# Kernel optimization log

Measured on AMD Instinct MI355X. Metric: run time of the kernel, lower is better.

## Reference

```python
import jax, jax.numpy as jnp
import numpy as np

B, T, D = 2, 2048, 1024
H, K = 16, 64  # num_heads, key_size (value_size == key_size)


def setup_inputs() -> dict:
    key = jax.random.key(0)
    ks = jax.random.split(key, 9)
    # xavier-uniform-ish scale for square-ish projections
    def xavier(k, shape):
        fan_in, fan_out = shape[0], shape[1]
        lim = jnp.sqrt(6.0 / (fan_in + fan_out))
        return jax.random.uniform(k, shape, jnp.float32, -lim, lim)
    return {
        "x_q": jax.random.normal(ks[0], (B, T, D), jnp.float32),
        "Wq": xavier(ks[1], (D, H * K)),
        "bq": jnp.zeros((H * K,), jnp.float32),
        "Wk": xavier(ks[2], (D, H * K)),
        "bk": jnp.zeros((H * K,), jnp.float32),
        "Wv": xavier(ks[3], (D, H * K)),
        "bv": jnp.zeros((H * K,), jnp.float32),
        "Wo": xavier(ks[4], (H * K, D)),
        "bo": jnp.zeros((D,), jnp.float32),
    }


def reference(x_q, Wq, bq, Wk, bk, Wv, bv, Wo, bo):
    # self-attention: x_k = x_v = x_q
    q = (x_q @ Wq + bq).reshape(B, T, H, K)
    k = (x_q @ Wk + bk).reshape(B, T, H, K)
    v = (x_q @ Wv + bv).reshape(B, T, H, K)
    # dense_dot_product_attention, mask=None
    logits = jnp.einsum('bqhd,bkhd->bhqk', q, k) / jnp.sqrt(jnp.asarray(K, k.dtype))
    attn_w = jax.nn.softmax(logits, axis=-1)  # [B,H,Tq,Tk]
    attn = jnp.einsum('bhqk,bkhd->bqhd', attn_w, v).reshape(B, T, H * K)
    out = attn @ Wo + bo  # [B,T,D]
    return out
```

## Files before the change

### kernel.cpp

```cpp
#include <hip/hip_runtime.h>
#include <hip/hip_bf16.h>
#include <stdint.h>

#define B_  2
#define T_  2048
#define D_  1024
#define H_  16
#define KS  64
#define M_  (B_*T_)

typedef unsigned short u16;
typedef __bf16 bf16x8 __attribute__((ext_vector_type(8)));
typedef __bf16 bf16x4 __attribute__((ext_vector_type(4)));
typedef float  f32x4  __attribute__((ext_vector_type(4)));

#define AS1 __attribute__((address_space(1)))
#define AS3 __attribute__((address_space(3)))

__device__ inline u16 f2bf(float x){
  union { float f; uint32_t u; } v; v.f = x;
  uint32_t r = (v.u + 0x7fffu + ((v.u >> 16) & 1u)) >> 16;
  return (u16)r;
}

__device__ inline void gl_lds16(const u16* g, u16* l){
  __builtin_amdgcn_global_load_lds((AS1 void*)(const_cast<u16*>(g)),
                                   (AS3 void*)l, 16, 0, 0);
}

__global__ __launch_bounds__(256) void k_cvt_x(const float* __restrict__ x,
                                               u16* __restrict__ xb){
  int i = blockIdx.x * 256 + threadIdx.x;
  float4 v = ((const float4*)x)[i];
  ushort4 o;
  o.x = f2bf(v.x); o.y = f2bf(v.y); o.z = f2bf(v.z); o.w = f2bf(v.w);
  ((ushort4*)xb)[i] = o;
}

__global__ __launch_bounds__(256) void k_tconv_w(const float* __restrict__ W0,
                                                 const float* __restrict__ W1,
                                                 const float* __restrict__ W2,
                                                 const float* __restrict__ W3,
                                                 u16* __restrict__ out){
  const float* W = (blockIdx.z==0)?W0:(blockIdx.z==1)?W1:(blockIdx.z==2)?W2:W3;
  u16* o = out + (size_t)blockIdx.z * 1024 * 1024;
  __shared__ float tile[32][33];
  int tx = threadIdx.x, ty = threadIdx.y;
  int kb = blockIdx.y * 32, nb = blockIdx.x * 32;
  for(int i=0;i<4;i++) tile[ty+8*i][tx] = W[(size_t)(kb+ty+8*i)*1024 + nb+tx];
  __syncthreads();
  for(int i=0;i<4;i++){
    int n = nb + ty + 8*i;
    o[(size_t)n*1024 + kb + tx] = f2bf(tile[tx][ty+8*i]);
  }
}

template<bool CT>
__device__ inline void qkv_core(const u16* __restrict__ xb, const u16* __restrict__ BT,
                                int m0, int n0, u16* Asm, u16* Bsm,
                                f32x4 (&acc)[4][4],
                                int lane, int wm, int wn){
  int l15 = lane & 15, l4 = lane >> 4;
  int t = wm*128 + wn*64 + lane;
  (void)t;
  int tid = threadIdx.x;
  int srow = tid >> 3, schunk = tid & 7;
  for(int kt=0; kt<16; ++kt){
    __syncthreads();
    int kb = kt * 64;
    for(int i=0;i<4;i++){
      int row = i*32 + srow;
      int gch = schunk ^ (row & 7);
      gl_lds16(xb + (size_t)(m0+row)*1024 + kb + gch*8, Asm + row*64 + schunk*8);
      gl_lds16(BT + (size_t)(n0+row)*1024 + kb + gch*8, Bsm + row*64 + schunk*8);
    }
    __syncthreads();
    for(int c=0;c<2;c++){
      bf16x8 af[4], bfr[4];
      for(int mt=0;mt<4;mt++){
        int row = wm*64 + mt*16 + l15;
        int idx = (row*64 + c*32 + l4*8) ^ ((row & 7) << 3);
        af[mt] = *(const bf16x8*)(Asm + idx);
      }
      for(int nt=0;nt<4;nt++){
        int row = wn*64 + nt*16 + l15;
        int idx = (row*64 + c*32 + l4*8) ^ ((row & 7) << 3);
        bfr[nt] = *(const bf16x8*)(Bsm + idx);
      }
      for(int mt=0;mt<4;mt++)
        for(int nt=0;nt<4;nt++){
          if(CT)
            acc[mt][nt] = __builtin_amdgcn_mfma_f32_16x16x32_bf16(bfr[nt], af[mt], acc[mt][nt], 0,0,0);
          else
            acc[mt][nt] = __builtin_amdgcn_mfma_f32_16x16x32_bf16(af[mt], bfr[nt], acc[mt][nt], 0,0,0);
        }
    }
  }
}

__global__ __launch_bounds__(256) void k_gemm_qkv(const u16* __restrict__ xb,
                                                  const u16* __restrict__ wt,
                                                  const float* __restrict__ bq,
                                                  const float* __restrict__ bk,
                                                  const float* __restrict__ bv,
                                                  u16* __restrict__ qkv,
                                                  u16* __restrict__ vt){
  int widx = blockIdx.x >> 3;
  int n0   = (blockIdx.x & 7) * 128;
  int m0   = blockIdx.y * 128;
  const u16* BT = wt + (size_t)widx * (1024*1024);
  const float* bias = (widx==0)?bq:(widx==1)?bk:bv;
  u16* out = qkv + (size_t)widx * (4*1024*1024);
  float oscale = (widx==0) ? 0.125f * 1.44269504088896f : 1.0f;

  __shared__ u16 Asm[128*64];
  __shared__ u16 Bsm[128*64];
  int t = threadIdx.x;
  int lane = t & 63, w = t >> 6, wm = w >> 1, wn = w & 1;
  int l15 = lane & 15, l4 = lane >> 4;
  f32x4 zero = {0.f,0.f,0.f,0.f};
  f32x4 acc[4][4];
  for(int i=0;i<4;i++) for(int j=0;j<4;j++) acc[i][j] = zero;

  if(widx < 2){
    qkv_core<true >(xb, BT, m0, n0, Asm, Bsm, acc, lane, wm, wn);
    for(int nt=0;nt<4;nt++){
      int nb = n0 + wn*64 + nt*16 + l4*4;
      float4 b4 = *(const float4*)&bias[nb];
      int h = nb >> 6, kk = nb & 63;
      for(int mt=0;mt<4;mt++){
        int m = m0 + wm*64 + mt*16 + l15;
        int b = m >> 11, tt = m & 2047;
        bf16x4 pk;
        pk[0] = (__bf16)((acc[mt][nt][0] + b4.x) * oscale);
        pk[1] = (__bf16)((acc[mt][nt][1] + b4.y) * oscale);
        pk[2] = (__bf16)((acc[mt][nt][2] + b4.z) * oscale);
        pk[3] = (__bf16)((acc[mt][nt][3] + b4.w) * oscale);
        *(bf16x4*)(out + (((size_t)(b*H_ + h)*T_ + tt) << 6) + kk) = pk;
      }
    }
  } else {
    qkv_core<false>(xb, BT, m0, n0, Asm, Bsm, acc, lane, wm, wn);
    for(int nt=0;nt<4;nt++){
      int nbase = n0 + wn*64 + nt*16 + l15;
      float bv_ = bias[nbase];
      int h = nbase >> 6, kk = nbase & 63;
      for(int mt=0;mt<4;mt++){
        int m = m0 + wm*64 + mt*16 + l4*4;
        int b = m >> 11, tt = m & 2047;
        bf16x4 pk;
        for(int r=0;r<4;r++) pk[r] = (__bf16)(acc[mt][nt][r] + bv_);
        *(bf16x4*)(vt + (((size_t)(b*H_ + h)*64 + kk)*T_) + tt) = pk;
      }
    }
  }
}

__global__ __launch_bounds__(256, 3) void k_attn(const u16* __restrict__ Q,
                                                 const u16* __restrict__ Kg,
                                                 const u16* __restrict__ VT,
                                                 u16* __restrict__ attn_out){
  int bx0 = blockIdx.x;
  int bx  = (bx0 & 7) * 128 + (bx0 >> 3);
  int qt = bx & 31, h = (bx >> 5) & 15, b = bx >> 9;
  int bh = b*H_ + h;
  const u16* Qh = Q  + (size_t)bh * T_ * 64;
  const u16* Kh = Kg + (size_t)bh * T_ * 64;
  const u16* Vh = VT + (size_t)bh * 64 * T_;
  __shared__ u16 Ksm[2][64*64];
  __shared__ u16 Vsm[2][64*64];
  __shared__ u16 Psm[4][16*64];
  int t = threadIdx.x, lane = t & 63, w = t >> 6;
  int l15 = lane & 15, l4 = lane >> 4;

  bf16x8 qf[2];
  int qrow = qt*64 + w*16 + l15;
  for(int c=0;c<2;c++)
    qf[c] = *(const bf16x8*)(Qh + (size_t)qrow*64 + c*32 + l4*8);

  bf16x8 ones;
  for(int j=0;j<8;j++) ones[j] = (__bf16)1.0f;

  f32x4 zero = {0.f,0.f,0.f,0.f};
  f32x4 accT[4];
  for(int g=0;g<4;g++) accT[g] = zero;
  f32x4 accL = zero;
  float m_r = -3.0e38f;

  int srow = t >> 3, schunk = t & 7;
  int gchS = schunk ^ (srow & 7);

  gl_lds16(Kh + (size_t)srow*64      + gchS*8, &Ksm[0][srow*64      + schunk*8]);
  gl_lds16(Kh + (size_t)(srow+32)*64 + gchS*8, &Ksm[0][(srow+32)*64 + schunk*8]);
  gl_lds16(Vh + (size_t)srow*T_      + gchS*8, &Vsm[0][srow*64      + schunk*8]);
  gl_lds16(Vh + (size_t)(srow+32)*T_ + gchS*8, &Vsm[0][(srow+32)*64 + schunk*8]);
  __syncthreads();

  auto body = [&](int tile, int cur){
    if(tile+1 < 32){
      int kvb = (tile+1)*64;
      gl_lds16(Kh + (size_t)(kvb+srow)*64    + gchS*8, &Ksm[cur^1][srow*64      + schunk*8]);
      gl_lds16(Kh + (size_t)(kvb+srow+32)*64 + gchS*8, &Ksm[cur^1][(srow+32)*64 + schunk*8]);
      gl_lds16(Vh + (size_t)srow*T_      + kvb + gchS*8, &Vsm[cur^1][srow*64      + schunk*8]);
      gl_lds16(Vh + (size_t)(srow+32)*T_ + kvb + gchS*8, &Vsm[cur^1][(srow+32)*64 + schunk*8]);
    }

    f32x4 s[4];
    for(int g=0;g<4;g++) s[g] = zero;
    __builtin_amdgcn_s_setprio(1);
    for(int c=0;c<2;c++){
      for(int g=0;g<4;g++){
        int row = g*16 + l15;
        int idx = (row*64 + c*32 + l4*8) ^ ((row & 7) << 3);
        bf16x8 kf = *(const bf16x8*)(&Ksm[cur][idx]);
        s[g] = __builtin_amdgcn_mfma_f32_16x16x32_bf16(kf, qf[c], s[g], 0,0,0);
      }
    }
    __builtin_amdgcn_s_setprio(0);

    float t0 = fmaxf(fmaxf(fmaxf(s[0][0], s[0][1]), s[0][2]), s[0][3]);
    float t1 = fmaxf(fmaxf(fmaxf(s[1][0], s[1][1]), s[1][2]), s[1][3]);
    float t2 = fmaxf(fmaxf(fmaxf(s[2][0], s[2][1]), s[2][2]), s[2][3]);
    float t3 = fmaxf(fmaxf(fmaxf(s[3][0], s[3][1]), s[3][2]), s[3][3]);
    float pmax = fmaxf(fmaxf(fmaxf(t0, t1), t2), t3);
    pmax = fmaxf(pmax, __shfl_xor(pmax, 16));
    pmax = fmaxf(pmax, __shfl_xor(pmax, 32));
    if(__any(pmax > m_r + 8.f)){
      float mnew  = fmaxf(m_r, pmax);
      float alpha = __builtin_amdgcn_exp2f(m_r - mnew);
      m_r = mnew;
      for(int g=0;g<4;g++){
        f32x4 a = accT[g];
        for(int r=0;r<4;r++) a[r] *= alpha;
        accT[g] = a;
      }
      for(int r=0;r<4;r++) accL[r] *= alpha;
    }
    for(int g=0;g<4;g++)
      for(int r=0;r<4;r++)
        s[g][r] = __builtin_amdgcn_exp2f(s[g][r] - m_r);

    for(int g=0;g<4;g++){
      bf16x4 pk;
      for(int r=0;r<4;r++) pk[r] = (__bf16)s[g][r];
      int idx = (l15*64 + g*16 + l4*4) ^ ((l15 & 7) << 3);
      *(bf16x4*)(&Psm[w][idx]) = pk;
    }

    __builtin_amdgcn_s_setprio(1);
    for(int c=0;c<2;c++){
      int idx_p = (l15*64 + c*32 + l4*8) ^ ((l15 & 7) << 3);
      bf16x8 pf = *(const bf16x8*)(&Psm[w][idx_p]);
      accL = __builtin_amdgcn_mfma_f32_16x16x32_bf16(ones, pf, accL, 0,0,0);
      for(int g=0;g<4;g++){
        int row = g*16 + l15;
        int idx = (row*64 + c*32 + l4*8) ^ ((row & 7) << 3);
        bf16x8 vf = *(const bf16x8*)(&Vsm[cur][idx]);
        accT[g] = __builtin_amdgcn_mfma_f32_16x16x32_bf16(vf, pf, accT[g], 0,0,0);
      }
    }
    __builtin_amdgcn_s_setprio(0);

    __syncthreads();
  };

  for(int t2=0; t2<16; ++t2){
    body(2*t2,   0);
    body(2*t2+1, 1);
  }

  float oinv = 1.0f / accL[0];
  int m = b*T_ + qt*64 + w*16 + l15;
  for(int g=0;g<4;g++){
    bf16x4 pk;
    for(int r=0;r<4;r++) pk[r] = (__bf16)(accT[g][r] * oinv);
    *(bf16x4*)(attn_out + (size_t)m*1024 + h*64 + g*16 + l4*4) = pk;
  }
}

__global__ __launch_bounds__(256) void k_gemm_out(const u16* __restrict__ A,
                                                  const u16* __restrict__ BT,
                                                  const float* __restrict__ bias,
                                                  float* __restrict__ out){
  int n0 = blockIdx.x * 128;
  int m0 = blockIdx.y * 64;
  __shared__ u16 Asm[64*64];
  __shared__ u16 Bsm[128*64];
  int t = threadIdx.x;
  int lane = t & 63, w = t >> 6, wm = w >> 1, wn = w & 1;
  int l15 = lane & 15, l4 = lane >> 4;
  f32x4 zero = {0.f,0.f,0.f,0.f};
  f32x4 acc[2][4];
  for(int i=0;i<2;i++) for(int j=0;j<4;j++) acc[i][j] = zero;
  int srow = t >> 3, schunk = t & 7;

  for(int kt=0; kt<16; ++kt){
    __syncthreads();
    int kb = kt * 64;
    for(int i=0;i<2;i++){
      int row = i*32 + srow;
      int gch = schunk ^ (row & 7);
      gl_lds16(A  + (size_t)(m0+row)*1024 + kb + gch*8, Asm + row*64 + schunk*8);
    }
    for(int i=0;i<4;i++){
      int row = i*32 + srow;
      int gch = schunk ^ (row & 7);
      gl_lds16(BT + (size_t)(n0+row)*1024 + kb + gch*8, Bsm + row*64 + schunk*8);
    }
    __syncthreads();
    for(int c=0;c<2;c++){
      bf16x8 af[2], bfr[4];
      for(int mt=0;mt<2;mt++){
        int row = wm*32 + mt*16 + l15;
        int idx = (row*64 + c*32 + l4*8) ^ ((row & 7) << 3);
        af[mt] = *(const bf16x8*)(Asm + idx);
      }
      for(int nt=0;nt<4;nt++){
        int row = wn*64 + nt*16 + l15;
        int idx = (row*64 + c*32 + l4*8) ^ ((row & 7) << 3);
        bfr[nt] = *(const bf16x8*)(Bsm + idx);
      }
      for(int mt=0;mt<2;mt++)
        for(int nt=0;nt<4;nt++)
          acc[mt][nt] = __builtin_amdgcn_mfma_f32_16x16x32_bf16(bfr[nt], af[mt], acc[mt][nt], 0,0,0);
    }
  }
  for(int nt=0;nt<4;nt++){
    int nb = n0 + wn*64 + nt*16 + l4*4;
    float4 b4 = *(const float4*)&bias[nb];
    for(int mt=0;mt<2;mt++){
      int m = m0 + wm*32 + mt*16 + l15;
      float4 o;
      o.x = acc[mt][nt][0] + b4.x;
      o.y = acc[mt][nt][1] + b4.y;
      o.z = acc[mt][nt][2] + b4.z;
      o.w = acc[mt][nt][3] + b4.w;
      *(float4*)&out[(size_t)m*1024 + nb] = o;
    }
  }
}

extern "C" void kernel_launch(void* const* d_in, const int* in_sizes, int n_in,
                              void* d_out, int out_size, void* d_ws, size_t ws_size,
                              hipStream_t stream){
  const float* x  = (const float*)d_in[0];
  const float* Wq = (const float*)d_in[1];
  const float* bq = (const float*)d_in[2];
  const float* Wk = (const float*)d_in[3];
  const float* bk = (const float*)d_in[4];
  const float* Wv = (const float*)d_in[5];
  const float* bv = (const float*)d_in[6];
  const float* Wo = (const float*)d_in[7];
  const float* bo = (const float*)d_in[8];
  float* out = (float*)d_out;
  char* ws = (char*)d_ws;

  u16* xb  = (u16*)(ws);
  u16* wt  = (u16*)(ws + (8u  << 20));
  u16* qkv = (u16*)(ws + (16u << 20));
  u16* vt  = (u16*)(ws + (40u << 20));
  u16* at  = (u16*)(ws + (48u << 20));

  k_cvt_x   <<<4096, 256, 0, stream>>>(x, xb);
  k_tconv_w <<<dim3(32,32,4), dim3(32,8), 0, stream>>>(Wq, Wk, Wv, Wo, wt);
  k_gemm_qkv<<<dim3(24,32), 256, 0, stream>>>(xb, wt, bq, bk, bv, qkv, vt);
  k_attn    <<<1024, 256, 0, stream>>>(qkv, qkv + (size_t)4*1024*1024, vt, at);
  k_gemm_out<<<dim3(8,64), 256, 0, stream>>>(at, wt + (size_t)3*1024*1024, bo, out);
}
```

Measured before the change: 206.5 us.

## Double attention query rows per wave, merge prep kernels, swizzle GEMM block order

Each attention wave now processes two 16-row query sub-tiles against every K/V tile, so each K/V fragment read from LDS feeds twice as many MFMAs and the grid halves to 512 blocks. Launch bounds drop to 2 blocks per SM to leave room for the extra registers. The x conversion and weight transpose kernels are merged into one launch. The QKV and output GEMMs remap block indices with a swizzle for better L2 locality. The price is higher register pressure and fewer resident waves in attention.

```diff
diff --git a/kernel.cpp b/kernel.cpp
--- a/kernel.cpp
+++ b/kernel.cpp
@@ -28,30 +28,35 @@
                                    (AS3 void*)l, 16, 0, 0);
 }
 
-__global__ __launch_bounds__(256) void k_cvt_x(const float* __restrict__ x,
-                                               u16* __restrict__ xb){
-  int i = blockIdx.x * 256 + threadIdx.x;
-  float4 v = ((const float4*)x)[i];
-  ushort4 o;
-  o.x = f2bf(v.x); o.y = f2bf(v.y); o.z = f2bf(v.z); o.w = f2bf(v.w);
-  ((ushort4*)xb)[i] = o;
-}
-
-__global__ __launch_bounds__(256) void k_tconv_w(const float* __restrict__ W0,
-                                                 const float* __restrict__ W1,
-                                                 const float* __restrict__ W2,
-                                                 const float* __restrict__ W3,
-                                                 u16* __restrict__ out){
-  const float* W = (blockIdx.z==0)?W0:(blockIdx.z==1)?W1:(blockIdx.z==2)?W2:W3;
-  u16* o = out + (size_t)blockIdx.z * 1024 * 1024;
-  __shared__ float tile[32][33];
-  int tx = threadIdx.x, ty = threadIdx.y;
-  int kb = blockIdx.y * 32, nb = blockIdx.x * 32;
-  for(int i=0;i<4;i++) tile[ty+8*i][tx] = W[(size_t)(kb+ty+8*i)*1024 + nb+tx];
-  __syncthreads();
-  for(int i=0;i<4;i++){
-    int n = nb + ty + 8*i;
-    o[(size_t)n*1024 + kb + tx] = f2bf(tile[tx][ty+8*i]);
+__global__ __launch_bounds__(256) void k_prep(const float* __restrict__ x,
+                                              u16* __restrict__ xb,
+                                              const float* __restrict__ W0,
+                                              const float* __restrict__ W1,
+                                              const float* __restrict__ W2,
+                                              const float* __restrict__ W3,
+                                              u16* __restrict__ wt){
+  int bid = blockIdx.x, tid = threadIdx.x;
+  if(bid < 4096){
+    int i = bid * 256 + tid;
+    float4 v = ((const float4*)x)[i];
+    ushort4 o;
+    o.x = f2bf(v.x); o.y = f2bf(v.y); o.z = f2bf(v.z); o.w = f2bf(v.w);
+    ((ushort4*)xb)[i] = o;
+  } else {
+    int pid = bid - 4096;
+    int z = pid >> 10, rem = pid & 1023;
+    int by = rem >> 5, bx = rem & 31;
+    const float* W = (z==0)?W0:(z==1)?W1:(z==2)?W2:W3;
+    u16* o = wt + (size_t)z * 1024 * 1024;
+    __shared__ float tile[32][33];
+    int tx = tid & 31, ty = tid >> 5;
+    int kb = by * 32, nb = bx * 32;
+    for(int i=0;i<4;i++) tile[ty+8*i][tx] = W[(size_t)(kb+ty+8*i)*1024 + nb+tx];
+    __syncthreads();
+    for(int i=0;i<4;i++){
+      int n = nb + ty + 8*i;
+      o[(size_t)n*1024 + kb + tx] = f2bf(tile[tx][ty+8*i]);
+    }
   }
 }
 
@@ -61,8 +66,6 @@
                                 f32x4 (&acc)[4][4],
                                 int lane, int wm, int wn){
   int l15 = lane & 15, l4 = lane >> 4;
-  int t = wm*128 + wn*64 + lane;
-  (void)t;
   int tid = threadIdx.x;
   int srow = tid >> 3, schunk = tid & 7;
   for(int kt=0; kt<16; ++kt){
@@ -105,9 +108,12 @@
                                                   const float* __restrict__ bv,
                                                   u16* __restrict__ qkv,
                                                   u16* __restrict__ vt){
-  int widx = blockIdx.x >> 3;
-  int n0   = (blockIdx.x & 7) * 128;
-  int m0   = blockIdx.y * 128;
+  int bid = blockIdx.x;
+  int sw  = (bid & 7) * 96 + (bid >> 3);
+  int mt_ = sw / 24, r = sw % 24;
+  int widx = r >> 3;
+  int n0   = (r & 7) * 128;
+  int m0   = mt_ * 128;
   const u16* BT = wt + (size_t)widx * (1024*1024);
   const float* bias = (widx==0)?bq:(widx==1)?bk:bv;
   u16* out = qkv + (size_t)widx * (4*1024*1024);
@@ -149,43 +155,45 @@
         int m = m0 + wm*64 + mt*16 + l4*4;
         int b = m >> 11, tt = m & 2047;
         bf16x4 pk;
-        for(int r=0;r<4;r++) pk[r] = (__bf16)(acc[mt][nt][r] + bv_);
+        for(int r2=0;r2<4;r2++) pk[r2] = (__bf16)(acc[mt][nt][r2] + bv_);
         *(bf16x4*)(vt + (((size_t)(b*H_ + h)*64 + kk)*T_) + tt) = pk;
       }
     }
   }
 }
 
-__global__ __launch_bounds__(256, 3) void k_attn(const u16* __restrict__ Q,
+__global__ __launch_bounds__(256, 2) void k_attn(const u16* __restrict__ Q,
                                                  const u16* __restrict__ Kg,
                                                  const u16* __restrict__ VT,
                                                  u16* __restrict__ attn_out){
   int bx0 = blockIdx.x;
-  int bx  = (bx0 & 7) * 128 + (bx0 >> 3);
-  int qt = bx & 31, h = (bx >> 5) & 15, b = bx >> 9;
+  int bx  = (bx0 & 7) * 64 + (bx0 >> 3);
+  int qt = bx & 15, h = (bx >> 4) & 15, b = bx >> 8;
   int bh = b*H_ + h;
   const u16* Qh = Q  + (size_t)bh * T_ * 64;
   const u16* Kh = Kg + (size_t)bh * T_ * 64;
   const u16* Vh = VT + (size_t)bh * 64 * T_;
   __shared__ u16 Ksm[2][64*64];
   __shared__ u16 Vsm[2][64*64];
-  __shared__ u16 Psm[4][16*64];
+  __shared__ u16 Psm[4][32*64];
   int t = threadIdx.x, lane = t & 63, w = t >> 6;
   int l15 = lane & 15, l4 = lane >> 4;
 
-  bf16x8 qf[2];
-  int qrow = qt*64 + w*16 + l15;
-  for(int c=0;c<2;c++)
-    qf[c] = *(const bf16x8*)(Qh + (size_t)qrow*64 + c*32 + l4*8);
+  bf16x8 qf[2][2];
+  for(int ss=0; ss<2; ++ss){
+    int qrow = qt*128 + w*32 + ss*16 + l15;
+    for(int c=0;c<2;c++)
+      qf[ss][c] = *(const bf16x8*)(Qh + (size_t)qrow*64 + c*32 + l4*8);
+  }
 
   bf16x8 ones;
   for(int j=0;j<8;j++) ones[j] = (__bf16)1.0f;
 
   f32x4 zero = {0.f,0.f,0.f,0.f};
-  f32x4 accT[4];
-  for(int g=0;g<4;g++) accT[g] = zero;
-  f32x4 accL = zero;
-  float m_r = -3.0e38f;
+  f32x4 accT[2][4];
+  for(int ss=0;ss<2;ss++) for(int g=0;g<4;g++) accT[ss][g] = zero;
+  f32x4 accL[2] = {zero, zero};
+  float m_r[2] = {-3.0e38f, -3.0e38f};
 
   int srow = t >> 3, schunk = t & 7;
   int gchS = schunk ^ (srow & 7);
@@ -205,58 +213,80 @@
       gl_lds16(Vh + (size_t)(srow+32)*T_ + kvb + gchS*8, &Vsm[cur^1][(srow+32)*64 + schunk*8]);
     }
 
-    f32x4 s[4];
-    for(int g=0;g<4;g++) s[g] = zero;
+    f32x4 s_[2][4];
+    for(int ss=0;ss<2;ss++) for(int g=0;g<4;g++) s_[ss][g] = zero;
     __builtin_amdgcn_s_setprio(1);
     for(int c=0;c<2;c++){
       for(int g=0;g<4;g++){
         int row = g*16 + l15;
         int idx = (row*64 + c*32 + l4*8) ^ ((row & 7) << 3);
         bf16x8 kf = *(const bf16x8*)(&Ksm[cur][idx]);
-        s[g] = __builtin_amdgcn_mfma_f32_16x16x32_bf16(kf, qf[c], s[g], 0,0,0);
+        s_[0][g] = __builtin_amdgcn_mfma_f32_16x16x32_bf16(kf, qf[0][c], s_[0][g], 0,0,0);
+        s_[1][g] = __builtin_amdgcn_mfma_f32_16x16x32_bf16(kf, qf[1][c], s_[1][g], 0,0,0);
       }
     }
     __builtin_amdgcn_s_setprio(0);
 
-    float t0 = fmaxf(fmaxf(fmaxf(s[0][0], s[0][1]), s[0][2]), s[0][3]);
-    float t1 = fmaxf(fmaxf(fmaxf(s[1][0], s[1][1]), s[1][2]), s[1][3]);
-    float t2 = fmaxf(fmaxf(fmaxf(s[2][0], s[2][1]), s[2][2]), s[2][3]);
-    float t3 = fmaxf(fmaxf(fmaxf(s[3][0], s[3][1]), s[3][2]), s[3][3]);
-    float pmax = fmaxf(fmaxf(fmaxf(t0, t1), t2), t3);
-    pmax = fmaxf(pmax, __shfl_xor(pmax, 16));
-    pmax = fmaxf(pmax, __shfl_xor(pmax, 32));
-    if(__any(pmax > m_r + 8.f)){
-      float mnew  = fmaxf(m_r, pmax);
-      float alpha = __builtin_amdgcn_exp2f(m_r - mnew);
-      m_r = mnew;
+    float pmax[2];
+    #pragma unroll
+    for(int ss=0;ss<2;ss++){
+      float t0 = fmaxf(fmaxf(fmaxf(s_[ss][0][0], s_[ss][0][1]), s_[ss][0][2]), s_[ss][0][3]);
+      float t1 = fmaxf(fmaxf(fmaxf(s_[ss][1][0], s_[ss][1][1]), s_[ss][1][2]), s_[ss][1][3]);
+      float t2 = fmaxf(fmaxf(fmaxf(s_[ss][2][0], s_[ss][2][1]), s_[ss][2][2]), s_[ss][2][3]);
+      float t3 = fmaxf(fmaxf(fmaxf(s_[ss][3][0], s_[ss][3][1]), s_[ss][3][2]), s_[ss][3][3]);
+      float p = fmaxf(fmaxf(fmaxf(t0, t1), t2), t3);
+      p = fmaxf(p, __shfl_xor(p, 16));
+      p = fmaxf(p, __shfl_xor(p, 32));
+      pmax[ss] = p;
+    }
+    if(__any(fmaxf(pmax[0] - m_r[0], pmax[1] - m_r[1]) > 8.f)){
+      #pragma unroll
+      for(int ss=0;ss<2;ss++){
+        float mnew  = fmaxf(m_r[ss], pmax[ss]);
+        float alpha = __builtin_amdgcn_exp2f(m_r[ss] - mnew);
+        m_r[ss] = mnew;
+        for(int g=0;g<4;g++){
+          f32x4 a = accT[ss][g];
+          for(int r=0;r<4;r++) a[r] *= alpha;
+          accT[ss][g] = a;
+        }
+        for(int r=0;r<4;r++) accL[ss][r] *= alpha;
+      }
+    }
+    #pragma unroll
+    for(int ss=0;ss<2;ss++)
+      for(int g=0;g<4;g++)
+        for(int r=0;r<4;r++)
+          s_[ss][g][r] = __builtin_amdgcn_exp2f(s_[ss][g][r] - m_r[ss]);
+
+    #pragma unroll
+    for(int ss=0;ss<2;ss++){
+      int row = ss*16 + l15;
       for(int g=0;g<4;g++){
-        f32x4 a = accT[g];
-        for(int r=0;r<4;r++) a[r] *= alpha;
-        accT[g] = a;
-      }
-      for(int r=0;r<4;r++) accL[r] *= alpha;
-    }
-    for(int g=0;g<4;g++)
-      for(int r=0;r<4;r++)
-        s[g][r] = __builtin_amdgcn_exp2f(s[g][r] - m_r);
-
-    for(int g=0;g<4;g++){
-      bf16x4 pk;
-      for(int r=0;r<4;r++) pk[r] = (__bf16)s[g][r];
-      int idx = (l15*64 + g*16 + l4*4) ^ ((l15 & 7) << 3);
-      *(bf16x4*)(&Psm[w][idx]) = pk;
+        bf16x4 pk;
+        for(int r=0;r<4;r++) pk[r] = (__bf16)s_[ss][g][r];
+        int idx = (row*64 + g*16 + l4*4) ^ ((row & 7) << 3);
+        *(bf16x4*)(&Psm[w][idx]) = pk;
+      }
     }
 
     __builtin_amdgcn_s_setprio(1);
     for(int c=0;c<2;c++){
-      int idx_p = (l15*64 + c*32 + l4*8) ^ ((l15 & 7) << 3);
-      bf16x8 pf = *(const bf16x8*)(&Psm[w][idx_p]);
-      accL = __builtin_amdgcn_mfma_f32_16x16x32_bf16(ones, pf, accL, 0,0,0);
+      bf16x8 pf0, pf1;
+      {
+        int row0 = l15,      idx0 = (row0*64 + c*32 + l4*8) ^ ((row0 & 7) << 3);
+        int row1 = 16 + l15, idx1 = (row1*64 + c*32 + l4*8) ^ ((row1 & 7) << 3);
+        pf0 = *(const bf16x8*)(&Psm[w][idx0]);
+        pf1 = *(const bf16x8*)(&Psm[w][idx1]);
+      }
+      accL[0] = __builtin_amdgcn_mfma_f32_16x16x32_bf16(ones, pf0, accL[0], 0,0,0);
+      accL[1] = __builtin_amdgcn_mfma_f32_16x16x32_bf16(ones, pf1, accL[1], 0,0,0);
       for(int g=0;g<4;g++){
         int row = g*16 + l15;
         int idx = (row*64 + c*32 + l4*8) ^ ((row & 7) << 3);
         bf16x8 vf = *(const bf16x8*)(&Vsm[cur][idx]);
-        accT[g] = __builtin_amdgcn_mfma_f32_16x16x32_bf16(vf, pf, accT[g], 0,0,0);
+        accT[0][g] = __builtin_amdgcn_mfma_f32_16x16x32_bf16(vf, pf0, accT[0][g], 0,0,0);
+        accT[1][g] = __builtin_amdgcn_mfma_f32_16x16x32_bf16(vf, pf1, accT[1][g], 0,0,0);
       }
     }
     __builtin_amdgcn_s_setprio(0);
@@ -269,12 +299,15 @@
     body(2*t2+1, 1);
   }
 
-  float oinv = 1.0f / accL[0];
-  int m = b*T_ + qt*64 + w*16 + l15;
-  for(int g=0;g<4;g++){
-    bf16x4 pk;
-    for(int r=0;r<4;r++) pk[r] = (__bf16)(accT[g][r] * oinv);
-    *(bf16x4*)(attn_out + (size_t)m*1024 + h*64 + g*16 + l4*4) = pk;
+  #pragma unroll
+  for(int ss=0;ss<2;ss++){
+    float oinv = 1.0f / accL[ss][0];
+    int m = b*T_ + qt*128 + w*32 + ss*16 + l15;
+    for(int g=0;g<4;g++){
+      bf16x4 pk;
+      for(int r=0;r<4;r++) pk[r] = (__bf16)(accT[ss][g][r] * oinv);
+      *(bf16x4*)(attn_out + (size_t)m*1024 + h*64 + g*16 + l4*4) = pk;
+    }
   }
 }
 
@@ -282,8 +315,10 @@
                                                   const u16* __restrict__ BT,
                                                   const float* __restrict__ bias,
                                                   float* __restrict__ out){
-  int n0 = blockIdx.x * 128;
-  int m0 = blockIdx.y * 64;
+  int bid = blockIdx.x;
+  int sw  = (bid & 7) * 64 + (bid >> 3);
+  int n0 = (sw & 7) * 128;
+  int m0 = (sw >> 3) * 64;
   __shared__ u16 Asm[64*64];
   __shared__ u16 Bsm[128*64];
   int t = threadIdx.x;
@@ -361,9 +396,8 @@
   u16* vt  = (u16*)(ws + (40u << 20));
   u16* at  = (u16*)(ws + (48u << 20));
 
-  k_cvt_x   <<<4096, 256, 0, stream>>>(x, xb);
-  k_tconv_w <<<dim3(32,32,4), dim3(32,8), 0, stream>>>(Wq, Wk, Wv, Wo, wt);
-  k_gemm_qkv<<<dim3(24,32), 256, 0, stream>>>(xb, wt, bq, bk, bv, qkv, vt);
-  k_attn    <<<1024, 256, 0, stream>>>(qkv, qkv + (size_t)4*1024*1024, vt, at);
-  k_gemm_out<<<dim3(8,64), 256, 0, stream>>>(at, wt + (size_t)3*1024*1024, bo, out);
-}
+  k_prep    <<<8192, 256, 0, stream>>>(x, xb, Wq, Wk, Wv, Wo, wt);
+  k_gemm_qkv<<<768,  256, 0, stream>>>(xb, wt, bq, bk, bv, qkv, vt);
+  k_attn    <<<512,  256, 0, stream>>>(qkv, qkv + (size_t)4*1024*1024, vt, at);
+  k_gemm_out<<<512,  256, 0, stream>>>(at, wt + (size_t)3*1024*1024, bo, out);
+}
```

New measurement: 201.1 us. 2.6% less time.
